# Optimization experiments

Measured on AMD Instinct MI355X. Metric: run time of the kernel, lower is better.

The kernel has to match this reference:

```python
import jax, jax.numpy as jnp
import numpy as np

B, N, DIM, H = 8, 2048, 64, 8  # per-head dim == DIM (module convention: inner_dim = dim * n_heads)


def setup_inputs() -> dict:
    key = jax.random.key(0)
    k1, k2, k3 = jax.random.split(key, 3)
    x = jax.random.normal(k1, (B, N, DIM), dtype=jnp.float32)
    W_qkv = jax.random.normal(k2, (DIM, 3 * H * DIM), dtype=jnp.float32) * (DIM ** -0.5)
    W_out = jax.random.normal(k3, (H * DIM, DIM), dtype=jnp.float32) * ((H * DIM) ** -0.5)
    b_out = jnp.zeros((DIM,), dtype=jnp.float32)
    return {"x": x, "W_qkv": W_qkv, "W_out": W_out, "b_out": b_out}


def reference(x, W_qkv, W_out, b_out):
    b, n, d = x.shape
    h = W_qkv.shape[1] // (3 * d)
    qkv = x @ W_qkv                                   # [b, n, 3*h*d]
    q, k, v = jnp.split(qkv, 3, axis=-1)              # each [b, n, h*d]
    def to_heads(t):
        return t.reshape(b, n, h, d).transpose(0, 2, 1, 3)  # [b, h, n, d]
    q, k, v = map(to_heads, (q, k, v))
    scale = d ** -0.5
    dot = jnp.einsum('bhid,bhjd->bhij', q, k) * scale  # [b, h, n, n]
    A = jax.nn.softmax(dot, axis=-1)
    z = jnp.einsum('bhij,bhjd->bhid', A, v)            # [b, h, n, d]
    z = z.transpose(0, 2, 1, 3).reshape(b, n, h * d)   # [b, n, h*d]
    return z @ W_out + b_out                           # [b, n, d]
```

## Files before the change

### kernel.cpp

```cpp
#include <hip/hip_runtime.h>
#include <math.h>

#define BB 8
#define NN 2048
#define DD 64
#define HH 8
#define BH (BB*HH)
#define HD (HH*DD)
#define NROWS (BB*NN)
#define QKV_COLS (3*HD)

typedef __bf16 bf16_8 __attribute__((ext_vector_type(8)));
typedef __bf16 bf16_4 __attribute__((ext_vector_type(4)));
typedef float  f32_16 __attribute__((ext_vector_type(16)));
typedef float  f32_4  __attribute__((ext_vector_type(4)));
typedef int    i32_2  __attribute__((ext_vector_type(2)));

#define QSCALE 0.180336880111f

__device__ __forceinline__ unsigned pack_bf16(float a, float b) {
  union { __bf16 h[2]; unsigned u; } t;
  t.h[0] = (__bf16)a; t.h[1] = (__bf16)b;
  return t.u;
}

__device__ __forceinline__ float fast_exp2(float x) {
#if __has_builtin(__builtin_amdgcn_exp2f)
  return __builtin_amdgcn_exp2f(x);
#else
  return __expf(x * 0.69314718056f);
#endif
}

__device__ __forceinline__ bf16_8 half_swap(unsigned a0, unsigned a1,
                                            unsigned a2, unsigned a3,
                                            int lhi, int xl) {
  union { unsigned u[4]; bf16_8 v; } F;
#if __has_builtin(__builtin_amdgcn_permlane32_swap)
  i32_2 r02 = __builtin_amdgcn_permlane32_swap((int)a0, (int)a2, false, false);
  i32_2 r13 = __builtin_amdgcn_permlane32_swap((int)a1, (int)a3, false, false);
  F.u[0] = (unsigned)r02.x; F.u[2] = (unsigned)r02.y;
  F.u[1] = (unsigned)r13.x; F.u[3] = (unsigned)r13.y;
#else
  unsigned w0 = (unsigned)__shfl((int)a0, xl, 64);
  unsigned w1 = (unsigned)__shfl((int)a1, xl, 64);
  unsigned w2 = (unsigned)__shfl((int)a2, xl, 64);
  unsigned w3 = (unsigned)__shfl((int)a3, xl, 64);
  F.u[0] = lhi ? w2 : a0;
  F.u[1] = lhi ? w3 : a1;
  F.u[2] = lhi ? a2 : w0;
  F.u[3] = lhi ? a3 : w1;
#endif
  return F.v;
}

__global__ __launch_bounds__(256) void qkv_kernel(
    const float* __restrict__ x, const float* __restrict__ Wqkv,
    const float* __restrict__ Wout,
    __bf16* __restrict__ Q, __bf16* __restrict__ K, __bf16* __restrict__ Vt,
    __bf16* __restrict__ Wob) {
  __shared__ __bf16 T[4][64][34];

  if (blockIdx.y == (NROWS / 128)) {
    int id = blockIdx.x * 256 + threadIdx.x;
    for (int e = id; e < 512 * 64; e += 24 * 256) {
      int kf = e >> 6, col = e & 63;
      int s = kf >> 4, lh = (kf >> 3) & 1, j = kf & 7;
      int t = col >> 5, lc = col & 31;
      Wob[((size_t)((t * 32 + s) * 64 + lh * 32 + lc)) * 8 + j] = (__bf16)Wout[e];
    }
    return;
  }

  const int lane = threadIdx.x & 63;
  const int wave = threadIdx.x >> 6;
  const int l31  = lane & 31, lhi = lane >> 5;
  const int cg   = blockIdx.x;
  const int row0 = blockIdx.y * 128 + wave * 32;

  const float* xr = x + (size_t)(row0 + l31) * 64 + lhi * 8;
  bf16_8 af[4];
#pragma unroll
  for (int s = 0; s < 4; s++) {
    f32_4 a0 = *(const f32_4*)(xr + s * 16);
    f32_4 a1 = *(const f32_4*)(xr + s * 16 + 4);
#pragma unroll
    for (int j = 0; j < 4; j++) { af[s][j] = (__bf16)a0[j]; af[s][4 + j] = (__bf16)a1[j]; }
  }

  const int col0  = cg * 64;
  const int which = col0 >> 9;
  const float wscl = (which == 0) ? QSCALE : 1.0f;

  f32_16 C0, C1;
#pragma unroll
  for (int i = 0; i < 16; i++) { C0[i] = 0.f; C1[i] = 0.f; }

#pragma unroll
  for (int s = 0; s < 4; s++) {
    bf16_8 b0, b1;
#pragma unroll
    for (int j = 0; j < 8; j++) {
      int k = s * 16 + lhi * 8 + j;
      b0[j] = (__bf16)(Wqkv[(size_t)k * QKV_COLS + col0 + l31]      * wscl);
      b1[j] = (__bf16)(Wqkv[(size_t)k * QKV_COLS + col0 + 32 + l31] * wscl);
    }
    C0 = __builtin_amdgcn_mfma_f32_32x32x16_bf16(af[s], b0, C0, 0, 0, 0);
    C1 = __builtin_amdgcn_mfma_f32_32x32x16_bf16(af[s], b1, C1, 0, 0, 0);
  }

  const int h   = (col0 >> 6) & 7;
  const int b   = row0 >> 11;
  const int n0l = row0 & 2047;

  if (which < 2) {
    __bf16* dst = (which == 0) ? Q : K;
#pragma unroll
    for (int r = 0; r < 16; r++) {
      int nl = (r & 3) + 8 * (r >> 2) + 4 * lhi;
      size_t base = (((size_t)(b * HH + h) * NN) + n0l + nl) * DD;
      dst[base + l31]      = (__bf16)C0[r];
      dst[base + 32 + l31] = (__bf16)C1[r];
    }
  } else {
    __bf16 (*Tw)[34] = T[wave];
#pragma unroll
    for (int r = 0; r < 16; r++) {
      int nl = (r & 3) + 8 * (r >> 2) + 4 * lhi;
      Tw[l31][nl]      = (__bf16)C0[r];
      Tw[32 + l31][nl] = (__bf16)C1[r];
    }
    __bf16* dst = Vt + (((size_t)(b * HH + h) * DD) + lane) * NN + n0l;
#pragma unroll
    for (int j = 0; j < 4; j++) {
      *(bf16_8*)(dst + j * 8) = *(const bf16_8*)(&Tw[lane][j * 8]);
    }
  }
}

#define TILE_ELEMS (128 * 72 + 64 * 136)
__global__ __launch_bounds__(512, 2) void attn_kernel(
    const __bf16* __restrict__ Q, const __bf16* __restrict__ K,
    const __bf16* __restrict__ Vt, __bf16* __restrict__ z) {
  __shared__ __bf16 SMEM[2][TILE_ELEMS];

  const int tid  = threadIdx.x;
  const int wave = tid >> 6;
  const int lane = tid & 63;
  const int l31  = lane & 31;
  const int lhi  = lane >> 5;
  const int xl   = lane ^ 32;
  const int bh   = blockIdx.x >> 2;
  const int q0   = (blockIdx.x & 3) * 512 + wave * 64;

  const __bf16* Qbase = Q + ((size_t)bh * NN + q0 + l31) * DD + lhi * 8;
  bf16_8 qfa[4], qfb[4];
#pragma unroll
  for (int s = 0; s < 4; s++) {
    qfa[s] = *(const bf16_8*)(Qbase + s * 16);
    qfb[s] = *(const bf16_8*)(Qbase + (size_t)32 * DD + s * 16);
  }

  f32_16 O0a, O1a, O0b, O1b;
#pragma unroll
  for (int i = 0; i < 16; i++) { O0a[i] = 0.f; O1a[i] = 0.f; O0b[i] = 0.f; O1b[i] = 0.f; }
  float lsa = 0.f, lsb = 0.f;

  const __bf16* Kb = K  + (size_t)bh * NN * DD;
  const __bf16* Vb = Vt + (size_t)bh * DD * NN;

  const int krow = tid >> 3, kcol = (tid & 7) * 8;
  const int vrow = tid >> 4, vcol = (tid & 15) * 8;
  const __bf16* kgl = Kb + (size_t)krow * 64 + kcol;
  const __bf16* vgl = Vb + (size_t)vrow * NN + vcol;
  const int koff0 = krow * 72 + kcol;
  const int voff0 = 128 * 72 + vrow * 136 + vcol;

  bf16_8 gk[2], gv[2];
#pragma unroll
  for (int i = 0; i < 2; i++) {
    gk[i] = *(const bf16_8*)(kgl + (size_t)i * 64 * 64);
    gv[i] = *(const bf16_8*)(vgl + (size_t)i * 32 * NN);
  }
  {
    __bf16* S = SMEM[0];
    *(bf16_8*)(S + koff0)            = gk[0];
    *(bf16_8*)(S + koff0 + 64 * 72)  = gk[1];
    *(bf16_8*)(S + voff0)            = gv[0];
    *(bf16_8*)(S + voff0 + 32 * 136) = gv[1];
  }
#pragma unroll
  for (int i = 0; i < 2; i++) {
    gk[i] = *(const bf16_8*)(kgl + (size_t)128 * 64 + (size_t)i * 64 * 64);
    gv[i] = *(const bf16_8*)(vgl + 128 + (size_t)i * 32 * NN);
  }
  __syncthreads();

  for (int it = 0; it < 16; it++) {
    __bf16* Ks = SMEM[it & 1];
    __bf16* Vs = SMEM[it & 1] + 128 * 72;

    if (it < 15) {
      __bf16* Sn = SMEM[(it + 1) & 1];
      *(bf16_8*)(Sn + koff0)            = gk[0];
      *(bf16_8*)(Sn + koff0 + 64 * 72)  = gk[1];
      *(bf16_8*)(Sn + voff0)            = gv[0];
      *(bf16_8*)(Sn + voff0 + 32 * 136) = gv[1];
      if (it < 14) {
        const size_t kadv = (size_t)(it + 2) * 128 * 64;
        const size_t vadv = (size_t)(it + 2) * 128;
#pragma unroll
        for (int i = 0; i < 2; i++) {
          gk[i] = *(const bf16_8*)(kgl + kadv + (size_t)i * 64 * 64);
          gv[i] = *(const bf16_8*)(vgl + vadv + (size_t)i * 32 * NN);
        }
      }
    }

#pragma unroll
    for (int grp = 0; grp < 4; grp++) {
      const int kb0 = grp * 32;

      f32_16 Sa, Sb;
#pragma unroll
      for (int i = 0; i < 16; i++) { Sa[i] = 0.f; Sb[i] = 0.f; }
#pragma unroll
      for (int s = 0; s < 4; s++) {
        bf16_8 kb = *(const bf16_8*)(&Ks[(kb0 + l31) * 72 + s * 16 + lhi * 8]);
        Sa = __builtin_amdgcn_mfma_f32_32x32x16_bf16(kb, qfa[s], Sa, 0, 0, 0);
        Sb = __builtin_amdgcn_mfma_f32_32x32x16_bf16(kb, qfb[s], Sb, 0, 0, 0);
      }

      unsigned pka[8], pkb[8];
#pragma unroll
      for (int t = 0; t < 8; t++) {
        float a0 = fast_exp2(Sa[2 * t]), a1 = fast_exp2(Sa[2 * t + 1]);
        lsa += a0 + a1;
        pka[t] = pack_bf16(a0, a1);
        float b0 = fast_exp2(Sb[2 * t]), b1 = fast_exp2(Sb[2 * t + 1]);
        lsb += b0 + b1;
        pkb[t] = pack_bf16(b0, b1);
      }

#pragma unroll
      for (int g = 0; g < 2; g++) {
        const int kc = kb0 + g * 16;
        bf16_8 va0 = *(const bf16_8*)(&Vs[l31 * 136 + kc + lhi * 8]);
        bf16_8 va1 = *(const bf16_8*)(&Vs[(32 + l31) * 136 + kc + lhi * 8]);
        bf16_8 Fa = half_swap(pka[g * 4], pka[g * 4 + 1], pka[g * 4 + 2], pka[g * 4 + 3], lhi, xl);
        O0a = __builtin_amdgcn_mfma_f32_32x32x16_bf16(va0, Fa, O0a, 0, 0, 0);
        O1a = __builtin_amdgcn_mfma_f32_32x32x16_bf16(va1, Fa, O1a, 0, 0, 0);
        bf16_8 Fb = half_swap(pkb[g * 4], pkb[g * 4 + 1], pkb[g * 4 + 2], pkb[g * 4 + 3], lhi, xl);
        O0b = __builtin_amdgcn_mfma_f32_32x32x16_bf16(va0, Fb, O0b, 0, 0, 0);
        O1b = __builtin_amdgcn_mfma_f32_32x32x16_bf16(va1, Fb, O1b, 0, 0, 0);
      }
    }
    __syncthreads();
  }

  lsa += __shfl_xor(lsa, 32, 64);
  lsb += __shfl_xor(lsb, 32, 64);
  const float inva = 1.f / lsa;
  const float invb = 1.f / lsb;

  const int b = bh >> 3, h = bh & 7;
  __bf16* ow = SMEM[0] + wave * (32 * 68);
  const int qr = lane >> 1, c0 = (lane & 1) * 32;
#pragma unroll
  for (int sub = 0; sub < 2; sub++) {
    const f32_16& P0 = sub ? O0b : O0a;
    const f32_16& P1 = sub ? O1b : O1a;
    const float inv = sub ? invb : inva;
#pragma unroll
    for (int g = 0; g < 4; g++) {
      bf16_4 p0, p1;
#pragma unroll
      for (int i = 0; i < 4; i++) {
        p0[i] = (__bf16)(P0[4 * g + i] * inv);
        p1[i] = (__bf16)(P1[4 * g + i] * inv);
      }
      const int d0 = 8 * g + 4 * lhi;
      *(bf16_4*)(ow + l31 * 68 + d0)      = p0;
      *(bf16_4*)(ow + l31 * 68 + 32 + d0) = p1;
    }
    __bf16* zp = z + ((size_t)b * NN + q0 + sub * 32 + qr) * HD + h * DD + c0;
#pragma unroll
    for (int j = 0; j < 4; j++) {
      *(bf16_8*)(zp + 8 * j) = *(const bf16_8*)(ow + qr * 68 + c0 + 8 * j);
    }
  }
}

__global__ __launch_bounds__(256) void out_proj_kernel(
    const __bf16* __restrict__ z, const __bf16* __restrict__ Wob,
    const float* __restrict__ bout, float* __restrict__ out) {
  __shared__ float red[3][64][33];
  const int tid  = threadIdx.x;
  const int wave = tid >> 6, lane = tid & 63;
  const int l31  = lane & 31, lhi = lane >> 5;
  const int row0 = blockIdx.x * 32;

  const __bf16* zr = z + (size_t)(row0 + l31) * HD + wave * 128 + lhi * 8;

  f32_16 C0, C1;
#pragma unroll
  for (int i = 0; i < 16; i++) { C0[i] = 0.f; C1[i] = 0.f; }

#pragma unroll
  for (int s = 0; s < 8; s++) {
    const int sa = wave * 8 + s;
    bf16_8 a  = *(const bf16_8*)(zr + s * 16);
    bf16_8 b0 = *(const bf16_8*)(Wob + ((size_t)((0 * 32 + sa) * 64 + lane)) * 8);
    bf16_8 b1 = *(const bf16_8*)(Wob + ((size_t)((1 * 32 + sa) * 64 + lane)) * 8);
    C0 = __builtin_amdgcn_mfma_f32_32x32x16_bf16(a, b0, C0, 0, 0, 0);
    C1 = __builtin_amdgcn_mfma_f32_32x32x16_bf16(a, b1, C1, 0, 0, 0);
  }

  if (wave) {
    float* rw = &red[wave - 1][lane][0];
#pragma unroll
    for (int r = 0; r < 16; r++) { rw[r] = C0[r]; rw[16 + r] = C1[r]; }
  }
  __syncthreads();
  if (wave == 0) {
    const float bi0 = bout[l31], bi1 = bout[32 + l31];
#pragma unroll
    for (int r = 0; r < 16; r++) {
      int n = row0 + (r & 3) + 8 * (r >> 2) + 4 * lhi;
      float v0 = C0[r] + red[0][lane][r]      + red[1][lane][r]      + red[2][lane][r];
      float v1 = C1[r] + red[0][lane][16 + r] + red[1][lane][16 + r] + red[2][lane][16 + r];
      out[(size_t)n * 64 + l31]      = v0 + bi0;
      out[(size_t)n * 64 + 32 + l31] = v1 + bi1;
    }
  }
}

extern "C" void kernel_launch(void* const* d_in, const int* in_sizes, int n_in,
                              void* d_out, int out_size, void* d_ws, size_t ws_size,
                              hipStream_t stream) {
  const float* x    = (const float*)d_in[0];
  const float* Wqkv = (const float*)d_in[1];
  const float* Wout = (const float*)d_in[2];
  const float* bout = (const float*)d_in[3];
  float* out = (float*)d_out;

  const size_t buf_elems = (size_t)BB * HH * NN * DD;
  __bf16* Qw  = (__bf16*)d_ws;
  __bf16* Kw  = Qw  + buf_elems;
  __bf16* Vtw = Kw  + buf_elems;
  __bf16* zw  = Vtw + buf_elems;
  __bf16* Wob = zw  + buf_elems;

  qkv_kernel<<<dim3(QKV_COLS / 64, NROWS / 128 + 1), 256, 0, stream>>>(
      x, Wqkv, Wout, Qw, Kw, Vtw, Wob);
  attn_kernel<<<BH * (NN / 512), 512, 0, stream>>>(Qw, Kw, Vtw, zw);
  out_proj_kernel<<<NROWS / 32, 256, 0, stream>>>(zw, Wob, bout, out);
}
```

Before: 168.8 us.

## Fuse output projection into attention epilogue with atomic accumulation, stage Q/K stores via LDS

Removes the separate out_proj kernel and the z intermediate buffer. Each attention wave multiplies its normalized per-head output by that head's slice of W_out using MFMA and atomically adds the result into a zeroed fp32 output, with the bias added only by head 0. This saves the z write/read round trip and one launch, at the cost of a memset, eight-way float atomic contention per output element, and non-deterministic summation order. It also stages Q/K stores in the qkv kernel through LDS so global writes become coalesced 16-byte vectors.

```diff
diff --git a/kernel.cpp b/kernel.cpp
--- a/kernel.cpp
+++ b/kernel.cpp
@@ -114,13 +114,20 @@
   const int n0l = row0 & 2047;
 
   if (which < 2) {
-    __bf16* dst = (which == 0) ? Q : K;
+    __bf16* Tw = &T[wave][0][0];
 #pragma unroll
     for (int r = 0; r < 16; r++) {
       int nl = (r & 3) + 8 * (r >> 2) + 4 * lhi;
-      size_t base = (((size_t)(b * HH + h) * NN) + n0l + nl) * DD;
-      dst[base + l31]      = (__bf16)C0[r];
-      dst[base + 32 + l31] = (__bf16)C1[r];
+      Tw[nl * 66 + l31]      = (__bf16)C0[r];
+      Tw[nl * 66 + 32 + l31] = (__bf16)C1[r];
+    }
+    __bf16* dstb = ((which == 0) ? Q : K) +
+                   (((size_t)(b * HH + h) * NN) + n0l) * DD;
+    const int qr = lane >> 1, c0 = (lane & 1) * 32;
+#pragma unroll
+    for (int j = 0; j < 4; j++) {
+      *(bf16_8*)(dstb + (size_t)qr * DD + c0 + 8 * j) =
+          *(const bf16_8*)(&Tw[qr * 66 + c0 + 8 * j]);
     }
   } else {
     __bf16 (*Tw)[34] = T[wave];
@@ -141,7 +148,8 @@
 #define TILE_ELEMS (128 * 72 + 64 * 136)
 __global__ __launch_bounds__(512, 2) void attn_kernel(
     const __bf16* __restrict__ Q, const __bf16* __restrict__ K,
-    const __bf16* __restrict__ Vt, __bf16* __restrict__ z) {
+    const __bf16* __restrict__ Vt, const __bf16* __restrict__ Wob,
+    const float* __restrict__ bout, float* __restrict__ out) {
   __shared__ __bf16 SMEM[2][TILE_ELEMS];
 
   const int tid  = threadIdx.x;
@@ -264,73 +272,41 @@
   const float invb = 1.f / lsb;
 
   const int b = bh >> 3, h = bh & 7;
-  __bf16* ow = SMEM[0] + wave * (32 * 68);
-  const int qr = lane >> 1, c0 = (lane & 1) * 32;
+  const float bi0 = (h == 0) ? bout[l31]      : 0.f;
+  const float bi1 = (h == 0) ? bout[32 + l31] : 0.f;
+
 #pragma unroll
   for (int sub = 0; sub < 2; sub++) {
     const f32_16& P0 = sub ? O0b : O0a;
     const f32_16& P1 = sub ? O1b : O1a;
     const float inv = sub ? invb : inva;
-#pragma unroll
-    for (int g = 0; g < 4; g++) {
-      bf16_4 p0, p1;
-#pragma unroll
-      for (int i = 0; i < 4; i++) {
-        p0[i] = (__bf16)(P0[4 * g + i] * inv);
-        p1[i] = (__bf16)(P1[4 * g + i] * inv);
-      }
-      const int d0 = 8 * g + 4 * lhi;
-      *(bf16_4*)(ow + l31 * 68 + d0)      = p0;
-      *(bf16_4*)(ow + l31 * 68 + 32 + d0) = p1;
-    }
-    __bf16* zp = z + ((size_t)b * NN + q0 + sub * 32 + qr) * HD + h * DD + c0;
-#pragma unroll
-    for (int j = 0; j < 4; j++) {
-      *(bf16_8*)(zp + 8 * j) = *(const bf16_8*)(ow + qr * 68 + c0 + 8 * j);
-    }
-  }
-}
-
-__global__ __launch_bounds__(256) void out_proj_kernel(
-    const __bf16* __restrict__ z, const __bf16* __restrict__ Wob,
-    const float* __restrict__ bout, float* __restrict__ out) {
-  __shared__ float red[3][64][33];
-  const int tid  = threadIdx.x;
-  const int wave = tid >> 6, lane = tid & 63;
-  const int l31  = lane & 31, lhi = lane >> 5;
-  const int row0 = blockIdx.x * 32;
-
-  const __bf16* zr = z + (size_t)(row0 + l31) * HD + wave * 128 + lhi * 8;
-
-  f32_16 C0, C1;
-#pragma unroll
-  for (int i = 0; i < 16; i++) { C0[i] = 0.f; C1[i] = 0.f; }
-
-#pragma unroll
-  for (int s = 0; s < 8; s++) {
-    const int sa = wave * 8 + s;
-    bf16_8 a  = *(const bf16_8*)(zr + s * 16);
-    bf16_8 b0 = *(const bf16_8*)(Wob + ((size_t)((0 * 32 + sa) * 64 + lane)) * 8);
-    bf16_8 b1 = *(const bf16_8*)(Wob + ((size_t)((1 * 32 + sa) * 64 + lane)) * 8);
-    C0 = __builtin_amdgcn_mfma_f32_32x32x16_bf16(a, b0, C0, 0, 0, 0);
-    C1 = __builtin_amdgcn_mfma_f32_32x32x16_bf16(a, b1, C1, 0, 0, 0);
-  }
-
-  if (wave) {
-    float* rw = &red[wave - 1][lane][0];
-#pragma unroll
-    for (int r = 0; r < 16; r++) { rw[r] = C0[r]; rw[16 + r] = C1[r]; }
-  }
-  __syncthreads();
-  if (wave == 0) {
-    const float bi0 = bout[l31], bi1 = bout[32 + l31];
+
+    unsigned ok[16];
+#pragma unroll
+    for (int t = 0; t < 8; t++) {
+      ok[t]     = pack_bf16(P0[2 * t] * inv, P0[2 * t + 1] * inv);
+      ok[8 + t] = pack_bf16(P1[2 * t] * inv, P1[2 * t + 1] * inv);
+    }
+
+    f32_16 D0, D1;
+#pragma unroll
+    for (int i = 0; i < 16; i++) { D0[i] = 0.f; D1[i] = 0.f; }
+#pragma unroll
+    for (int s = 0; s < 4; s++) {
+      const int base = (s >> 1) * 8 + (s & 1) * 4;
+      bf16_8 F = half_swap(ok[base], ok[base + 1], ok[base + 2], ok[base + 3], lhi, xl);
+      bf16_8 w0 = *(const bf16_8*)(Wob + ((size_t)((0 * 32 + h * 4 + s) * 64 + lane)) * 8);
+      bf16_8 w1 = *(const bf16_8*)(Wob + ((size_t)((1 * 32 + h * 4 + s) * 64 + lane)) * 8);
+      D0 = __builtin_amdgcn_mfma_f32_32x32x16_bf16(F, w0, D0, 0, 0, 0);
+      D1 = __builtin_amdgcn_mfma_f32_32x32x16_bf16(F, w1, D1, 0, 0, 0);
+    }
+
+    float* ob = out + ((size_t)b * NN + q0 + sub * 32) * 64;
 #pragma unroll
     for (int r = 0; r < 16; r++) {
-      int n = row0 + (r & 3) + 8 * (r >> 2) + 4 * lhi;
-      float v0 = C0[r] + red[0][lane][r]      + red[1][lane][r]      + red[2][lane][r];
-      float v1 = C1[r] + red[0][lane][16 + r] + red[1][lane][16 + r] + red[2][lane][16 + r];
-      out[(size_t)n * 64 + l31]      = v0 + bi0;
-      out[(size_t)n * 64 + 32 + l31] = v1 + bi1;
+      int qr = (r & 3) + 8 * (r >> 2) + 4 * lhi;
+      atomicAdd(&ob[(size_t)qr * 64 + l31],      D0[r] + bi0);
+      atomicAdd(&ob[(size_t)qr * 64 + 32 + l31], D1[r] + bi1);
     }
   }
 }
@@ -348,11 +324,10 @@
   __bf16* Qw  = (__bf16*)d_ws;
   __bf16* Kw  = Qw  + buf_elems;
   __bf16* Vtw = Kw  + buf_elems;
-  __bf16* zw  = Vtw + buf_elems;
-  __bf16* Wob = zw  + buf_elems;
-
+  __bf16* Wob = Vtw + buf_elems;
+
+  hipMemsetAsync(out, 0, (size_t)NROWS * DD * sizeof(float), stream);
   qkv_kernel<<<dim3(QKV_COLS / 64, NROWS / 128 + 1), 256, 0, stream>>>(
       x, Wqkv, Wout, Qw, Kw, Vtw, Wob);
-  attn_kernel<<<BH * (NN / 512), 512, 0, stream>>>(Qw, Kw, Vtw, zw);
-  out_proj_kernel<<<NROWS / 32, 256, 0, stream>>>(zw, Wob, bout, out);
-}
+  attn_kernel<<<BH * (NN / 512), 512, 0, stream>>>(Qw, Kw, Vtw, Wob, bout, out);
+}
```

After: 186.4 us. 1.1x slower.

## Pretranspose QKV weights to bf16 and reuse x fragments across column groups

Applied to the files above, without the earlier changes.

Adds a small prep kernel that converts W_qkv to bf16, applies the Q scale once, and transposes it to column-major so each lane can load 8 contiguous bf16 values. The same kernel also builds the W_out layout. The QKV projection grid shrinks from 24 column groups to 4, and each block loops over 6 column groups, reusing the x fragments it already converted. This removes strided fp32 weight loads with per-element conversion and repeated x loads, at the cost of an extra kernel launch and less parallelism per block.

```diff
diff --git a/kernel.cpp b/kernel.cpp
--- a/kernel.cpp
+++ b/kernel.cpp
@@ -54,29 +54,35 @@
   return F.v;
 }
 
+__global__ __launch_bounds__(256) void wprep_kernel(
+    const float* __restrict__ Wqkv, const float* __restrict__ Wout,
+    __bf16* __restrict__ Wtq, __bf16* __restrict__ Wob) {
+  int idx = blockIdx.x * 256 + threadIdx.x;
+  if (idx < 64 * QKV_COLS) {
+    int k = idx / QKV_COLS, col = idx % QKV_COLS;
+    float v = Wqkv[idx];
+    if (col < HD) v *= QSCALE;
+    Wtq[(size_t)col * 64 + k] = (__bf16)v;
+  } else {
+    int e = idx - 64 * QKV_COLS;
+    int kf = e >> 6, col = e & 63;
+    int s = kf >> 4, lh = (kf >> 3) & 1, j = kf & 7;
+    int t = col >> 5, lc = col & 31;
+    Wob[((size_t)((t * 32 + s) * 64 + lh * 32 + lc)) * 8 + j] = (__bf16)Wout[e];
+  }
+}
+
 __global__ __launch_bounds__(256) void qkv_kernel(
-    const float* __restrict__ x, const float* __restrict__ Wqkv,
-    const float* __restrict__ Wout,
-    __bf16* __restrict__ Q, __bf16* __restrict__ K, __bf16* __restrict__ Vt,
-    __bf16* __restrict__ Wob) {
+    const float* __restrict__ x, const __bf16* __restrict__ Wtq,
+    __bf16* __restrict__ Q, __bf16* __restrict__ K, __bf16* __restrict__ Vt) {
   __shared__ __bf16 T[4][64][34];
-
-  if (blockIdx.y == (NROWS / 128)) {
-    int id = blockIdx.x * 256 + threadIdx.x;
-    for (int e = id; e < 512 * 64; e += 24 * 256) {
-      int kf = e >> 6, col = e & 63;
-      int s = kf >> 4, lh = (kf >> 3) & 1, j = kf & 7;
-      int t = col >> 5, lc = col & 31;
-      Wob[((size_t)((t * 32 + s) * 64 + lh * 32 + lc)) * 8 + j] = (__bf16)Wout[e];
-    }
-    return;
-  }
 
   const int lane = threadIdx.x & 63;
   const int wave = threadIdx.x >> 6;
   const int l31  = lane & 31, lhi = lane >> 5;
-  const int cg   = blockIdx.x;
   const int row0 = blockIdx.y * 128 + wave * 32;
+  const int b    = row0 >> 11;
+  const int n0l  = row0 & 2047;
 
   const float* xr = x + (size_t)(row0 + l31) * 64 + lhi * 8;
   bf16_8 af[4];
@@ -88,52 +94,46 @@
     for (int j = 0; j < 4; j++) { af[s][j] = (__bf16)a0[j]; af[s][4 + j] = (__bf16)a1[j]; }
   }
 
-  const int col0  = cg * 64;
-  const int which = col0 >> 9;
-  const float wscl = (which == 0) ? QSCALE : 1.0f;
-
-  f32_16 C0, C1;
-#pragma unroll
-  for (int i = 0; i < 16; i++) { C0[i] = 0.f; C1[i] = 0.f; }
-
-#pragma unroll
-  for (int s = 0; s < 4; s++) {
-    bf16_8 b0, b1;
-#pragma unroll
-    for (int j = 0; j < 8; j++) {
-      int k = s * 16 + lhi * 8 + j;
-      b0[j] = (__bf16)(Wqkv[(size_t)k * QKV_COLS + col0 + l31]      * wscl);
-      b1[j] = (__bf16)(Wqkv[(size_t)k * QKV_COLS + col0 + 32 + l31] * wscl);
-    }
-    C0 = __builtin_amdgcn_mfma_f32_32x32x16_bf16(af[s], b0, C0, 0, 0, 0);
-    C1 = __builtin_amdgcn_mfma_f32_32x32x16_bf16(af[s], b1, C1, 0, 0, 0);
-  }
-
-  const int h   = (col0 >> 6) & 7;
-  const int b   = row0 >> 11;
-  const int n0l = row0 & 2047;
-
-  if (which < 2) {
-    __bf16* dst = (which == 0) ? Q : K;
-#pragma unroll
-    for (int r = 0; r < 16; r++) {
-      int nl = (r & 3) + 8 * (r >> 2) + 4 * lhi;
-      size_t base = (((size_t)(b * HH + h) * NN) + n0l + nl) * DD;
-      dst[base + l31]      = (__bf16)C0[r];
-      dst[base + 32 + l31] = (__bf16)C1[r];
-    }
-  } else {
-    __bf16 (*Tw)[34] = T[wave];
-#pragma unroll
-    for (int r = 0; r < 16; r++) {
-      int nl = (r & 3) + 8 * (r >> 2) + 4 * lhi;
-      Tw[l31][nl]      = (__bf16)C0[r];
-      Tw[32 + l31][nl] = (__bf16)C1[r];
-    }
-    __bf16* dst = Vt + (((size_t)(b * HH + h) * DD) + lane) * NN + n0l;
-#pragma unroll
-    for (int j = 0; j < 4; j++) {
-      *(bf16_8*)(dst + j * 8) = *(const bf16_8*)(&Tw[lane][j * 8]);
+  for (int i = 0; i < 6; i++) {
+    const int cg = blockIdx.x * 6 + i;
+    const __bf16* wb = Wtq + (size_t)cg * 64 * 64 + lhi * 8;
+
+    f32_16 C0, C1;
+#pragma unroll
+    for (int q = 0; q < 16; q++) { C0[q] = 0.f; C1[q] = 0.f; }
+#pragma unroll
+    for (int s = 0; s < 4; s++) {
+      bf16_8 b0 = *(const bf16_8*)(wb + (size_t)l31 * 64 + s * 16);
+      bf16_8 b1 = *(const bf16_8*)(wb + (size_t)(32 + l31) * 64 + s * 16);
+      C0 = __builtin_amdgcn_mfma_f32_32x32x16_bf16(af[s], b0, C0, 0, 0, 0);
+      C1 = __builtin_amdgcn_mfma_f32_32x32x16_bf16(af[s], b1, C1, 0, 0, 0);
+    }
+
+    const int which = cg >> 3;
+    const int h     = cg & 7;
+
+    if (which < 2) {
+      __bf16* dst = (which == 0) ? Q : K;
+#pragma unroll
+      for (int r = 0; r < 16; r++) {
+        int nl = (r & 3) + 8 * (r >> 2) + 4 * lhi;
+        size_t base = (((size_t)(b * HH + h) * NN) + n0l + nl) * DD;
+        dst[base + l31]      = (__bf16)C0[r];
+        dst[base + 32 + l31] = (__bf16)C1[r];
+      }
+    } else {
+      __bf16 (*Tw)[34] = T[wave];
+#pragma unroll
+      for (int r = 0; r < 16; r++) {
+        int nl = (r & 3) + 8 * (r >> 2) + 4 * lhi;
+        Tw[l31][nl]      = (__bf16)C0[r];
+        Tw[32 + l31][nl] = (__bf16)C1[r];
+      }
+      __bf16* dst = Vt + (((size_t)(b * HH + h) * DD) + lane) * NN + n0l;
+#pragma unroll
+      for (int j = 0; j < 4; j++) {
+        *(bf16_8*)(dst + j * 8) = *(const bf16_8*)(&Tw[lane][j * 8]);
+      }
     }
   }
 }
@@ -349,10 +349,11 @@
   __bf16* Kw  = Qw  + buf_elems;
   __bf16* Vtw = Kw  + buf_elems;
   __bf16* zw  = Vtw + buf_elems;
-  __bf16* Wob = zw  + buf_elems;
-
-  qkv_kernel<<<dim3(QKV_COLS / 64, NROWS / 128 + 1), 256, 0, stream>>>(
-      x, Wqkv, Wout, Qw, Kw, Vtw, Wob);
+  __bf16* Wtq = zw  + buf_elems;
+  __bf16* Wob = Wtq + (size_t)QKV_COLS * 64;
+
+  wprep_kernel<<<512, 256, 0, stream>>>(Wqkv, Wout, Wtq, Wob);
+  qkv_kernel<<<dim3(4, NROWS / 128), 256, 0, stream>>>(x, Wtq, Qw, Kw, Vtw);
   attn_kernel<<<BH * (NN / 512), 512, 0, stream>>>(Qw, Kw, Vtw, zw);
   out_proj_kernel<<<NROWS / 32, 256, 0, stream>>>(zw, Wob, bout, out);
 }
```

Result: slower. 179.6 us (+6.4%).

## Fuse QKV, attention and output projection into one persistent kernel with grid barriers

Applied to the files above, without the earlier changes.

Merges the three kernel launches into a single 256-block persistent kernel. Software grid barriers, built from atomic counters that are cleared by a memset, separate the QKV projection, attention and output projection phases. This removes launch overhead and the gaps between kernels. In exchange it adds a memset launch and the cost of the grid barriers, and it depends on all 256 blocks being co-resident (2 per CU), otherwise the kernel deadlocks. Per-phase parallelism is also fixed to 256 blocks.

```diff
diff --git a/kernel.cpp b/kernel.cpp
--- a/kernel.cpp
+++ b/kernel.cpp
@@ -54,95 +54,34 @@
   return F.v;
 }
 
-__global__ __launch_bounds__(256) void qkv_kernel(
+__device__ __forceinline__ void grid_barrier(unsigned* cnt, unsigned* gate) {
+  __syncthreads();
+  if (threadIdx.x == 0) {
+    __threadfence();
+    unsigned old = atomicAdd(cnt, 1u);
+    if (old == gridDim.x - 1) {
+      atomicExch(gate, 1u);
+    } else {
+      while (atomicAdd(gate, 0u) == 0u) {
+#if __has_builtin(__builtin_amdgcn_s_sleep)
+        __builtin_amdgcn_s_sleep(8);
+#endif
+      }
+    }
+    __threadfence();
+  }
+  __syncthreads();
+}
+
+#define TILE_ELEMS (128 * 72 + 64 * 136)
+
+__global__ __launch_bounds__(512, 2) void mha_mega(
     const float* __restrict__ x, const float* __restrict__ Wqkv,
-    const float* __restrict__ Wout,
+    const float* __restrict__ Wout, const float* __restrict__ bout,
     __bf16* __restrict__ Q, __bf16* __restrict__ K, __bf16* __restrict__ Vt,
-    __bf16* __restrict__ Wob) {
-  __shared__ __bf16 T[4][64][34];
-
-  if (blockIdx.y == (NROWS / 128)) {
-    int id = blockIdx.x * 256 + threadIdx.x;
-    for (int e = id; e < 512 * 64; e += 24 * 256) {
-      int kf = e >> 6, col = e & 63;
-      int s = kf >> 4, lh = (kf >> 3) & 1, j = kf & 7;
-      int t = col >> 5, lc = col & 31;
-      Wob[((size_t)((t * 32 + s) * 64 + lh * 32 + lc)) * 8 + j] = (__bf16)Wout[e];
-    }
-    return;
-  }
-
-  const int lane = threadIdx.x & 63;
-  const int wave = threadIdx.x >> 6;
-  const int l31  = lane & 31, lhi = lane >> 5;
-  const int cg   = blockIdx.x;
-  const int row0 = blockIdx.y * 128 + wave * 32;
-
-  const float* xr = x + (size_t)(row0 + l31) * 64 + lhi * 8;
-  bf16_8 af[4];
-#pragma unroll
-  for (int s = 0; s < 4; s++) {
-    f32_4 a0 = *(const f32_4*)(xr + s * 16);
-    f32_4 a1 = *(const f32_4*)(xr + s * 16 + 4);
-#pragma unroll
-    for (int j = 0; j < 4; j++) { af[s][j] = (__bf16)a0[j]; af[s][4 + j] = (__bf16)a1[j]; }
-  }
-
-  const int col0  = cg * 64;
-  const int which = col0 >> 9;
-  const float wscl = (which == 0) ? QSCALE : 1.0f;
-
-  f32_16 C0, C1;
-#pragma unroll
-  for (int i = 0; i < 16; i++) { C0[i] = 0.f; C1[i] = 0.f; }
-
-#pragma unroll
-  for (int s = 0; s < 4; s++) {
-    bf16_8 b0, b1;
-#pragma unroll
-    for (int j = 0; j < 8; j++) {
-      int k = s * 16 + lhi * 8 + j;
-      b0[j] = (__bf16)(Wqkv[(size_t)k * QKV_COLS + col0 + l31]      * wscl);
-      b1[j] = (__bf16)(Wqkv[(size_t)k * QKV_COLS + col0 + 32 + l31] * wscl);
-    }
-    C0 = __builtin_amdgcn_mfma_f32_32x32x16_bf16(af[s], b0, C0, 0, 0, 0);
-    C1 = __builtin_amdgcn_mfma_f32_32x32x16_bf16(af[s], b1, C1, 0, 0, 0);
-  }
-
-  const int h   = (col0 >> 6) & 7;
-  const int b   = row0 >> 11;
-  const int n0l = row0 & 2047;
-
-  if (which < 2) {
-    __bf16* dst = (which == 0) ? Q : K;
-#pragma unroll
-    for (int r = 0; r < 16; r++) {
-      int nl = (r & 3) + 8 * (r >> 2) + 4 * lhi;
-      size_t base = (((size_t)(b * HH + h) * NN) + n0l + nl) * DD;
-      dst[base + l31]      = (__bf16)C0[r];
-      dst[base + 32 + l31] = (__bf16)C1[r];
-    }
-  } else {
-    __bf16 (*Tw)[34] = T[wave];
-#pragma unroll
-    for (int r = 0; r < 16; r++) {
-      int nl = (r & 3) + 8 * (r >> 2) + 4 * lhi;
-      Tw[l31][nl]      = (__bf16)C0[r];
-      Tw[32 + l31][nl] = (__bf16)C1[r];
-    }
-    __bf16* dst = Vt + (((size_t)(b * HH + h) * DD) + lane) * NN + n0l;
-#pragma unroll
-    for (int j = 0; j < 4; j++) {
-      *(bf16_8*)(dst + j * 8) = *(const bf16_8*)(&Tw[lane][j * 8]);
-    }
-  }
-}
-
-#define TILE_ELEMS (128 * 72 + 64 * 136)
-__global__ __launch_bounds__(512, 2) void attn_kernel(
-    const __bf16* __restrict__ Q, const __bf16* __restrict__ K,
-    const __bf16* __restrict__ Vt, __bf16* __restrict__ z) {
-  __shared__ __bf16 SMEM[2][TILE_ELEMS];
+    __bf16* __restrict__ z, __bf16* __restrict__ Wob,
+    float* __restrict__ out, unsigned* __restrict__ bar) {
+  __shared__ __align__(16) unsigned char SMEMRAW[2 * TILE_ELEMS * 2];
 
   const int tid  = threadIdx.x;
   const int wave = tid >> 6;
@@ -150,187 +89,269 @@
   const int l31  = lane & 31;
   const int lhi  = lane >> 5;
   const int xl   = lane ^ 32;
-  const int bh   = blockIdx.x >> 2;
-  const int q0   = (blockIdx.x & 3) * 512 + wave * 64;
-
-  const __bf16* Qbase = Q + ((size_t)bh * NN + q0 + l31) * DD + lhi * 8;
-  bf16_8 qfa[4], qfb[4];
-#pragma unroll
-  for (int s = 0; s < 4; s++) {
-    qfa[s] = *(const bf16_8*)(Qbase + s * 16);
-    qfb[s] = *(const bf16_8*)(Qbase + (size_t)32 * DD + s * 16);
+
+  {
+    int gid = blockIdx.x * 512 + tid;
+    if (gid < 512 * 64) {
+      int kf = gid >> 6, col = gid & 63;
+      int s = kf >> 4, lh = (kf >> 3) & 1, j = kf & 7;
+      int t = col >> 5, lc = col & 31;
+      Wob[((size_t)((t * 32 + s) * 64 + lh * 32 + lc)) * 8 + j] = (__bf16)Wout[gid];
+    }
+
+    __bf16* Tq = (__bf16*)SMEMRAW + wave * (64 * 34);
+    const int gwave = blockIdx.x * 8 + wave;
+
+#pragma unroll 1
+    for (int t = 0; t < 6; t++) {
+      const int task = t * 2048 + gwave;
+      const int cg   = task >> 9;
+      const int row0 = (task & 511) * 32;
+
+      const float* xr = x + (size_t)(row0 + l31) * 64 + lhi * 8;
+      bf16_8 af[4];
+#pragma unroll
+      for (int s = 0; s < 4; s++) {
+        f32_4 a0 = *(const f32_4*)(xr + s * 16);
+        f32_4 a1 = *(const f32_4*)(xr + s * 16 + 4);
+#pragma unroll
+        for (int j = 0; j < 4; j++) { af[s][j] = (__bf16)a0[j]; af[s][4 + j] = (__bf16)a1[j]; }
+      }
+
+      const int col0  = cg * 64;
+      const int which = col0 >> 9;
+      const float wscl = (which == 0) ? QSCALE : 1.0f;
+
+      f32_16 C0, C1;
+#pragma unroll
+      for (int q = 0; q < 16; q++) { C0[q] = 0.f; C1[q] = 0.f; }
+
+#pragma unroll
+      for (int s = 0; s < 4; s++) {
+        bf16_8 b0, b1;
+#pragma unroll
+        for (int j = 0; j < 8; j++) {
+          int k = s * 16 + lhi * 8 + j;
+          b0[j] = (__bf16)(Wqkv[(size_t)k * QKV_COLS + col0 + l31]      * wscl);
+          b1[j] = (__bf16)(Wqkv[(size_t)k * QKV_COLS + col0 + 32 + l31] * wscl);
+        }
+        C0 = __builtin_amdgcn_mfma_f32_32x32x16_bf16(af[s], b0, C0, 0, 0, 0);
+        C1 = __builtin_amdgcn_mfma_f32_32x32x16_bf16(af[s], b1, C1, 0, 0, 0);
+      }
+
+      const int h   = (col0 >> 6) & 7;
+      const int bb  = row0 >> 11;
+      const int n0l = row0 & 2047;
+
+      if (which < 2) {
+        __bf16* dst = (which == 0) ? Q : K;
+#pragma unroll
+        for (int r = 0; r < 16; r++) {
+          int nl = (r & 3) + 8 * (r >> 2) + 4 * lhi;
+          size_t base = (((size_t)(bb * HH + h) * NN) + n0l + nl) * DD;
+          dst[base + l31]      = (__bf16)C0[r];
+          dst[base + 32 + l31] = (__bf16)C1[r];
+        }
+      } else {
+#pragma unroll
+        for (int r = 0; r < 16; r++) {
+          int nl = (r & 3) + 8 * (r >> 2) + 4 * lhi;
+          Tq[l31 * 34 + nl]        = (__bf16)C0[r];
+          Tq[(32 + l31) * 34 + nl] = (__bf16)C1[r];
+        }
+        __bf16* dst = Vt + (((size_t)(bb * HH + h) * DD) + lane) * NN + n0l;
+#pragma unroll
+        for (int j = 0; j < 4; j++) {
+          *(bf16_8*)(dst + j * 8) = *(const bf16_8*)(&Tq[lane * 34 + j * 8]);
+        }
+      }
+    }
   }
 
-  f32_16 O0a, O1a, O0b, O1b;
-#pragma unroll
-  for (int i = 0; i < 16; i++) { O0a[i] = 0.f; O1a[i] = 0.f; O0b[i] = 0.f; O1b[i] = 0.f; }
-  float lsa = 0.f, lsb = 0.f;
-
-  const __bf16* Kb = K  + (size_t)bh * NN * DD;
-  const __bf16* Vb = Vt + (size_t)bh * DD * NN;
-
-  const int krow = tid >> 3, kcol = (tid & 7) * 8;
-  const int vrow = tid >> 4, vcol = (tid & 15) * 8;
-  const __bf16* kgl = Kb + (size_t)krow * 64 + kcol;
-  const __bf16* vgl = Vb + (size_t)vrow * NN + vcol;
-  const int koff0 = krow * 72 + kcol;
-  const int voff0 = 128 * 72 + vrow * 136 + vcol;
-
-  bf16_8 gk[2], gv[2];
-#pragma unroll
-  for (int i = 0; i < 2; i++) {
-    gk[i] = *(const bf16_8*)(kgl + (size_t)i * 64 * 64);
-    gv[i] = *(const bf16_8*)(vgl + (size_t)i * 32 * NN);
+  grid_barrier(&bar[0], &bar[1]);
+
+  {
+    __bf16 (*SMEM)[TILE_ELEMS] = (__bf16 (*)[TILE_ELEMS])SMEMRAW;
+    const int bh = blockIdx.x >> 2;
+    const int q0 = (blockIdx.x & 3) * 512 + wave * 64;
+
+    const __bf16* Qbase = Q + ((size_t)bh * NN + q0 + l31) * DD + lhi * 8;
+    bf16_8 qfa[4], qfb[4];
+#pragma unroll
+    for (int s = 0; s < 4; s++) {
+      qfa[s] = *(const bf16_8*)(Qbase + s * 16);
+      qfb[s] = *(const bf16_8*)(Qbase + (size_t)32 * DD + s * 16);
+    }
+
+    f32_16 O0a, O1a, O0b, O1b;
+#pragma unroll
+    for (int i = 0; i < 16; i++) { O0a[i] = 0.f; O1a[i] = 0.f; O0b[i] = 0.f; O1b[i] = 0.f; }
+    float lsa = 0.f, lsb = 0.f;
+
+    const __bf16* Kb = K  + (size_t)bh * NN * DD;
+    const __bf16* Vb = Vt + (size_t)bh * DD * NN;
+
+    const int krow = tid >> 3, kcol = (tid & 7) * 8;
+    const int vrow = tid >> 4, vcol = (tid & 15) * 8;
+    const __bf16* kgl = Kb + (size_t)krow * 64 + kcol;
+    const __bf16* vgl = Vb + (size_t)vrow * NN + vcol;
+    const int koff0 = krow * 72 + kcol;
+    const int voff0 = 128 * 72 + vrow * 136 + vcol;
+
+    bf16_8 gk[2], gv[2];
+#pragma unroll
+    for (int i = 0; i < 2; i++) {
+      gk[i] = *(const bf16_8*)(kgl + (size_t)i * 64 * 64);
+      gv[i] = *(const bf16_8*)(vgl + (size_t)i * 32 * NN);
+    }
+    {
+      __bf16* S = SMEM[0];
+      *(bf16_8*)(S + koff0)            = gk[0];
+      *(bf16_8*)(S + koff0 + 64 * 72)  = gk[1];
+      *(bf16_8*)(S + voff0)            = gv[0];
+      *(bf16_8*)(S + voff0 + 32 * 136) = gv[1];
+    }
+#pragma unroll
+    for (int i = 0; i < 2; i++) {
+      gk[i] = *(const bf16_8*)(kgl + (size_t)128 * 64 + (size_t)i * 64 * 64);
+      gv[i] = *(const bf16_8*)(vgl + 128 + (size_t)i * 32 * NN);
+    }
+    __syncthreads();
+
+    for (int it = 0; it < 16; it++) {
+      __bf16* Ks = SMEM[it & 1];
+      __bf16* Vs = SMEM[it & 1] + 128 * 72;
+
+      if (it < 15) {
+        __bf16* Sn = SMEM[(it + 1) & 1];
+        *(bf16_8*)(Sn + koff0)            = gk[0];
+        *(bf16_8*)(Sn + koff0 + 64 * 72)  = gk[1];
+        *(bf16_8*)(Sn + voff0)            = gv[0];
+        *(bf16_8*)(Sn + voff0 + 32 * 136) = gv[1];
+        if (it < 14) {
+          const size_t kadv = (size_t)(it + 2) * 128 * 64;
+          const size_t vadv = (size_t)(it + 2) * 128;
+#pragma unroll
+          for (int i = 0; i < 2; i++) {
+            gk[i] = *(const bf16_8*)(kgl + kadv + (size_t)i * 64 * 64);
+            gv[i] = *(const bf16_8*)(vgl + vadv + (size_t)i * 32 * NN);
+          }
+        }
+      }
+
+#pragma unroll
+      for (int grp = 0; grp < 4; grp++) {
+        const int kb0 = grp * 32;
+
+        f32_16 Sa, Sb;
+#pragma unroll
+        for (int i = 0; i < 16; i++) { Sa[i] = 0.f; Sb[i] = 0.f; }
+#pragma unroll
+        for (int s = 0; s < 4; s++) {
+          bf16_8 kb = *(const bf16_8*)(&Ks[(kb0 + l31) * 72 + s * 16 + lhi * 8]);
+          Sa = __builtin_amdgcn_mfma_f32_32x32x16_bf16(kb, qfa[s], Sa, 0, 0, 0);
+          Sb = __builtin_amdgcn_mfma_f32_32x32x16_bf16(kb, qfb[s], Sb, 0, 0, 0);
+        }
+
+        unsigned pka[8], pkb[8];
+#pragma unroll
+        for (int t = 0; t < 8; t++) {
+          float a0 = fast_exp2(Sa[2 * t]), a1 = fast_exp2(Sa[2 * t + 1]);
+          lsa += a0 + a1;
+          pka[t] = pack_bf16(a0, a1);
+          float b0 = fast_exp2(Sb[2 * t]), b1 = fast_exp2(Sb[2 * t + 1]);
+          lsb += b0 + b1;
+          pkb[t] = pack_bf16(b0, b1);
+        }
+
+#pragma unroll
+        for (int g = 0; g < 2; g++) {
+          const int kc = kb0 + g * 16;
+          bf16_8 va0 = *(const bf16_8*)(&Vs[l31 * 136 + kc + lhi * 8]);
+          bf16_8 va1 = *(const bf16_8*)(&Vs[(32 + l31) * 136 + kc + lhi * 8]);
+          bf16_8 Fa = half_swap(pka[g * 4], pka[g * 4 + 1], pka[g * 4 + 2], pka[g * 4 + 3], lhi, xl);
+          O0a = __builtin_amdgcn_mfma_f32_32x32x16_bf16(va0, Fa, O0a, 0, 0, 0);
+          O1a = __builtin_amdgcn_mfma_f32_32x32x16_bf16(va1, Fa, O1a, 0, 0, 0);
+          bf16_8 Fb = half_swap(pkb[g * 4], pkb[g * 4 + 1], pkb[g * 4 + 2], pkb[g * 4 + 3], lhi, xl);
+          O0b = __builtin_amdgcn_mfma_f32_32x32x16_bf16(va0, Fb, O0b, 0, 0, 0);
+          O1b = __builtin_amdgcn_mfma_f32_32x32x16_bf16(va1, Fb, O1b, 0, 0, 0);
+        }
+      }
+      __syncthreads();
+    }
+
+    lsa += __shfl_xor(lsa, 32, 64);
+    lsb += __shfl_xor(lsb, 32, 64);
+    const float inva = 1.f / lsa;
+    const float invb = 1.f / lsb;
+
+    const int bb = bh >> 3, h = bh & 7;
+    __bf16* ow = SMEM[0] + wave * (32 * 68);
+    const int qr = lane >> 1, c0 = (lane & 1) * 32;
+#pragma unroll
+    for (int sub = 0; sub < 2; sub++) {
+      const f32_16& P0 = sub ? O0b : O0a;
+      const f32_16& P1 = sub ? O1b : O1a;
+      const float inv = sub ? invb : inva;
+#pragma unroll
+      for (int g = 0; g < 4; g++) {
+        bf16_4 p0, p1;
+#pragma unroll
+        for (int i = 0; i < 4; i++) {
+          p0[i] = (__bf16)(P0[4 * g + i] * inv);
+          p1[i] = (__bf16)(P1[4 * g + i] * inv);
+        }
+        const int d0 = 8 * g + 4 * lhi;
+        *(bf16_4*)(ow + l31 * 68 + d0)      = p0;
+        *(bf16_4*)(ow + l31 * 68 + 32 + d0) = p1;
+      }
+      __bf16* zp = z + ((size_t)bb * NN + q0 + sub * 32 + qr) * HD + h * DD + c0;
+#pragma unroll
+      for (int j = 0; j < 4; j++) {
+        *(bf16_8*)(zp + 8 * j) = *(const bf16_8*)(ow + qr * 68 + c0 + 8 * j);
+      }
+    }
   }
+
+  grid_barrier(&bar[2], &bar[3]);
+
   {
-    __bf16* S = SMEM[0];
-    *(bf16_8*)(S + koff0)            = gk[0];
-    *(bf16_8*)(S + koff0 + 64 * 72)  = gk[1];
-    *(bf16_8*)(S + voff0)            = gv[0];
-    *(bf16_8*)(S + voff0 + 32 * 136) = gv[1];
-  }
-#pragma unroll
-  for (int i = 0; i < 2; i++) {
-    gk[i] = *(const bf16_8*)(kgl + (size_t)128 * 64 + (size_t)i * 64 * 64);
-    gv[i] = *(const bf16_8*)(vgl + 128 + (size_t)i * 32 * NN);
-  }
-  __syncthreads();
-
-  for (int it = 0; it < 16; it++) {
-    __bf16* Ks = SMEM[it & 1];
-    __bf16* Vs = SMEM[it & 1] + 128 * 72;
-
-    if (it < 15) {
-      __bf16* Sn = SMEM[(it + 1) & 1];
-      *(bf16_8*)(Sn + koff0)            = gk[0];
-      *(bf16_8*)(Sn + koff0 + 64 * 72)  = gk[1];
-      *(bf16_8*)(Sn + voff0)            = gv[0];
-      *(bf16_8*)(Sn + voff0 + 32 * 136) = gv[1];
-      if (it < 14) {
-        const size_t kadv = (size_t)(it + 2) * 128 * 64;
-        const size_t vadv = (size_t)(it + 2) * 128;
-#pragma unroll
-        for (int i = 0; i < 2; i++) {
-          gk[i] = *(const bf16_8*)(kgl + kadv + (size_t)i * 64 * 64);
-          gv[i] = *(const bf16_8*)(vgl + vadv + (size_t)i * 32 * NN);
-        }
-      }
-    }
-
-#pragma unroll
-    for (int grp = 0; grp < 4; grp++) {
-      const int kb0 = grp * 32;
-
-      f32_16 Sa, Sb;
-#pragma unroll
-      for (int i = 0; i < 16; i++) { Sa[i] = 0.f; Sb[i] = 0.f; }
-#pragma unroll
-      for (int s = 0; s < 4; s++) {
-        bf16_8 kb = *(const bf16_8*)(&Ks[(kb0 + l31) * 72 + s * 16 + lhi * 8]);
-        Sa = __builtin_amdgcn_mfma_f32_32x32x16_bf16(kb, qfa[s], Sa, 0, 0, 0);
-        Sb = __builtin_amdgcn_mfma_f32_32x32x16_bf16(kb, qfb[s], Sb, 0, 0, 0);
-      }
-
-      unsigned pka[8], pkb[8];
-#pragma unroll
-      for (int t = 0; t < 8; t++) {
-        float a0 = fast_exp2(Sa[2 * t]), a1 = fast_exp2(Sa[2 * t + 1]);
-        lsa += a0 + a1;
-        pka[t] = pack_bf16(a0, a1);
-        float b0 = fast_exp2(Sb[2 * t]), b1 = fast_exp2(Sb[2 * t + 1]);
-        lsb += b0 + b1;
-        pkb[t] = pack_bf16(b0, b1);
-      }
-
-#pragma unroll
-      for (int g = 0; g < 2; g++) {
-        const int kc = kb0 + g * 16;
-        bf16_8 va0 = *(const bf16_8*)(&Vs[l31 * 136 + kc + lhi * 8]);
-        bf16_8 va1 = *(const bf16_8*)(&Vs[(32 + l31) * 136 + kc + lhi * 8]);
-        bf16_8 Fa = half_swap(pka[g * 4], pka[g * 4 + 1], pka[g * 4 + 2], pka[g * 4 + 3], lhi, xl);
-        O0a = __builtin_amdgcn_mfma_f32_32x32x16_bf16(va0, Fa, O0a, 0, 0, 0);
-        O1a = __builtin_amdgcn_mfma_f32_32x32x16_bf16(va1, Fa, O1a, 0, 0, 0);
-        bf16_8 Fb = half_swap(pkb[g * 4], pkb[g * 4 + 1], pkb[g * 4 + 2], pkb[g * 4 + 3], lhi, xl);
-        O0b = __builtin_amdgcn_mfma_f32_32x32x16_bf16(va0, Fb, O0b, 0, 0, 0);
-        O1b = __builtin_amdgcn_mfma_f32_32x32x16_bf16(va1, Fb, O1b, 0, 0, 0);
-      }
+    const int sb = wave >> 2, w4 = wave & 3;
+    const int row0 = (blockIdx.x * 2 + sb) * 32;
+    float (*red)[64][33] = (float (*)[64][33])(SMEMRAW + sb * 25344);
+
+    const __bf16* zr = z + (size_t)(row0 + l31) * HD + w4 * 128 + lhi * 8;
+
+    f32_16 C0, C1;
+#pragma unroll
+    for (int i = 0; i < 16; i++) { C0[i] = 0.f; C1[i] = 0.f; }
+
+#pragma unroll
+    for (int s = 0; s < 8; s++) {
+      const int sa = w4 * 8 + s;
+      bf16_8 a  = *(const bf16_8*)(zr + s * 16);
+      bf16_8 b0 = *(const bf16_8*)(Wob + ((size_t)((0 * 32 + sa) * 64 + lane)) * 8);
+      bf16_8 b1 = *(const bf16_8*)(Wob + ((size_t)((1 * 32 + sa) * 64 + lane)) * 8);
+      C0 = __builtin_amdgcn_mfma_f32_32x32x16_bf16(a, b0, C0, 0, 0, 0);
+      C1 = __builtin_amdgcn_mfma_f32_32x32x16_bf16(a, b1, C1, 0, 0, 0);
+    }
+
+    if (w4) {
+      float* rw = &red[w4 - 1][lane][0];
+#pragma unroll
+      for (int r = 0; r < 16; r++) { rw[r] = C0[r]; rw[16 + r] = C1[r]; }
     }
     __syncthreads();
-  }
-
-  lsa += __shfl_xor(lsa, 32, 64);
-  lsb += __shfl_xor(lsb, 32, 64);
-  const float inva = 1.f / lsa;
-  const float invb = 1.f / lsb;
-
-  const int b = bh >> 3, h = bh & 7;
-  __bf16* ow = SMEM[0] + wave * (32 * 68);
-  const int qr = lane >> 1, c0 = (lane & 1) * 32;
-#pragma unroll
-  for (int sub = 0; sub < 2; sub++) {
-    const f32_16& P0 = sub ? O0b : O0a;
-    const f32_16& P1 = sub ? O1b : O1a;
-    const float inv = sub ? invb : inva;
-#pragma unroll
-    for (int g = 0; g < 4; g++) {
-      bf16_4 p0, p1;
-#pragma unroll
-      for (int i = 0; i < 4; i++) {
-        p0[i] = (__bf16)(P0[4 * g + i] * inv);
-        p1[i] = (__bf16)(P1[4 * g + i] * inv);
-      }
-      const int d0 = 8 * g + 4 * lhi;
-      *(bf16_4*)(ow + l31 * 68 + d0)      = p0;
-      *(bf16_4*)(ow + l31 * 68 + 32 + d0) = p1;
-    }
-    __bf16* zp = z + ((size_t)b * NN + q0 + sub * 32 + qr) * HD + h * DD + c0;
-#pragma unroll
-    for (int j = 0; j < 4; j++) {
-      *(bf16_8*)(zp + 8 * j) = *(const bf16_8*)(ow + qr * 68 + c0 + 8 * j);
-    }
-  }
-}
-
-__global__ __launch_bounds__(256) void out_proj_kernel(
-    const __bf16* __restrict__ z, const __bf16* __restrict__ Wob,
-    const float* __restrict__ bout, float* __restrict__ out) {
-  __shared__ float red[3][64][33];
-  const int tid  = threadIdx.x;
-  const int wave = tid >> 6, lane = tid & 63;
-  const int l31  = lane & 31, lhi = lane >> 5;
-  const int row0 = blockIdx.x * 32;
-
-  const __bf16* zr = z + (size_t)(row0 + l31) * HD + wave * 128 + lhi * 8;
-
-  f32_16 C0, C1;
-#pragma unroll
-  for (int i = 0; i < 16; i++) { C0[i] = 0.f; C1[i] = 0.f; }
-
-#pragma unroll
-  for (int s = 0; s < 8; s++) {
-    const int sa = wave * 8 + s;
-    bf16_8 a  = *(const bf16_8*)(zr + s * 16);
-    bf16_8 b0 = *(const bf16_8*)(Wob + ((size_t)((0 * 32 + sa) * 64 + lane)) * 8);
-    bf16_8 b1 = *(const bf16_8*)(Wob + ((size_t)((1 * 32 + sa) * 64 + lane)) * 8);
-    C0 = __builtin_amdgcn_mfma_f32_32x32x16_bf16(a, b0, C0, 0, 0, 0);
-    C1 = __builtin_amdgcn_mfma_f32_32x32x16_bf16(a, b1, C1, 0, 0, 0);
-  }
-
-  if (wave) {
-    float* rw = &red[wave - 1][lane][0];
-#pragma unroll
-    for (int r = 0; r < 16; r++) { rw[r] = C0[r]; rw[16 + r] = C1[r]; }
-  }
-  __syncthreads();
-  if (wave == 0) {
-    const float bi0 = bout[l31], bi1 = bout[32 + l31];
-#pragma unroll
-    for (int r = 0; r < 16; r++) {
-      int n = row0 + (r & 3) + 8 * (r >> 2) + 4 * lhi;
-      float v0 = C0[r] + red[0][lane][r]      + red[1][lane][r]      + red[2][lane][r];
-      float v1 = C1[r] + red[0][lane][16 + r] + red[1][lane][16 + r] + red[2][lane][16 + r];
-      out[(size_t)n * 64 + l31]      = v0 + bi0;
-      out[(size_t)n * 64 + 32 + l31] = v1 + bi1;
+    if (w4 == 0) {
+      const float bi0 = bout[l31], bi1 = bout[32 + l31];
+#pragma unroll
+      for (int r = 0; r < 16; r++) {
+        int n = row0 + (r & 3) + 8 * (r >> 2) + 4 * lhi;
+        float v0 = C0[r] + red[0][lane][r]      + red[1][lane][r]      + red[2][lane][r];
+        float v1 = C1[r] + red[0][lane][16 + r] + red[1][lane][16 + r] + red[2][lane][16 + r];
+        out[(size_t)n * 64 + l31]      = v0 + bi0;
+        out[(size_t)n * 64 + 32 + l31] = v1 + bi1;
+      }
     }
   }
 }
@@ -350,9 +371,9 @@
   __bf16* Vtw = Kw  + buf_elems;
   __bf16* zw  = Vtw + buf_elems;
   __bf16* Wob = zw  + buf_elems;
-
-  qkv_kernel<<<dim3(QKV_COLS / 64, NROWS / 128 + 1), 256, 0, stream>>>(
-      x, Wqkv, Wout, Qw, Kw, Vtw, Wob);
-  attn_kernel<<<BH * (NN / 512), 512, 0, stream>>>(Qw, Kw, Vtw, zw);
-  out_proj_kernel<<<NROWS / 32, 256, 0, stream>>>(zw, Wob, bout, out);
-}
+  unsigned* bar = (unsigned*)(Wob + 32768);
+
+  hipMemsetAsync(bar, 0, 64, stream);
+  mha_mega<<<256, 512, 0, stream>>>(x, Wqkv, Wout, bout,
+                                    Qw, Kw, Vtw, zw, Wob, out, bar);
+}
```

After: 228.1 us. +35.2%, slower.
